# Performance work log

Measured on AMD Instinct MI355X. Metric: run time of the kernel, lower is better.

## Reference

```python
import jax, jax.numpy as jnp
import numpy as np

N_CODES = 1024
CODE_DIM = 64
COMMITMENT_WEIGHT = 0.5
DECAY = 0.99
EPSILON = 1e-05
TEMP = 1.0


def setup_inputs() -> dict:
    key = jax.random.key(0)
    k_z, k_e = jax.random.split(key)
    z = jax.random.normal(k_z, (8, 16384, CODE_DIM), dtype=jnp.float32)
    # xavier_uniform init for embedding [n_codes, code_dim]
    limit = float(np.sqrt(6.0 / (N_CODES + CODE_DIM)))
    embedding = jax.random.uniform(k_e, (N_CODES, CODE_DIM), dtype=jnp.float32,
                                   minval=-limit, maxval=limit)
    ema_cluster_size = jnp.zeros((N_CODES,), dtype=jnp.float32)
    ema_w = embedding.copy()
    return {"z": z, "embedding": embedding,
            "ema_cluster_size": ema_cluster_size, "ema_w": ema_w}


def reference(z, embedding, ema_cluster_size, ema_w):
    lead_shape = z.shape[:-1]
    zf = z.reshape(-1, z.shape[-1])  # [N, D]
    # squared-euclidean distances: ||z||^2 + ||e||^2 - 2 z e^T  -> [N, n_codes]
    d = (jnp.sum(zf * zf, axis=-1, keepdims=True)
         + jnp.sum(embedding * embedding, axis=-1)
         - 2.0 * (zf @ embedding.T)) / TEMP
    idx = jnp.argmin(d, axis=-1)  # [N]
    z_q_f = embedding[idx]        # [N, D]

    # --- EMA codebook update (no-grad buffer math) ---
    ones = jnp.ones_like(idx, dtype=zf.dtype)
    cluster_size = jax.ops.segment_sum(ones, idx, num_segments=N_CODES)      # one_hot.sum(0)
    new_ecs = ema_cluster_size * DECAY + (1.0 - DECAY) * cluster_size
    n = jnp.sum(new_ecs)
    cs = jnp.clip((new_ecs + EPSILON) / (n + N_CODES * EPSILON) * n, 0.01)
    dw = jax.ops.segment_sum(zf, idx, num_segments=N_CODES)                  # one_hot.T @ z
    new_ema_w = ema_w * DECAY + (1.0 - DECAY) * dw
    new_embedding = new_ema_w / cs[:, None]

    # --- losses (straight-through) ---
    z_q = z_q_f.reshape(z.shape)
    commitment_loss = jnp.mean((jax.lax.stop_gradient(z_q) - z) ** 2)
    codebook_loss = jnp.mean((z_q - jax.lax.stop_gradient(z)) ** 2)
    loss = commitment_loss * COMMITMENT_WEIGHT + codebook_loss
    z_q_st = z + jax.lax.stop_gradient(z_q - z)

    # --- perplexity (no-grad) ---
    avg_probs = cluster_size / jnp.sum(cluster_size)
    avg_probs = jnp.clip(avg_probs, 1e-10)
    avg_probs = avg_probs / jnp.sum(avg_probs)
    perplexity = jnp.exp(-jnp.sum(avg_probs * jnp.log(avg_probs)))

    encoding_indices = idx.reshape(lead_shape)
    return (z_q_st, encoding_indices, loss, perplexity,
            new_embedding, new_ecs, new_ema_w)
```

## Files before the change

### kernel.cpp

```cpp
#include <hip/hip_runtime.h>
#include <hip/hip_bf16.h>
#include <math.h>

#define N_ROWS   131072
#define DIMS     64
#define NCODES   1024
#define DECAY    0.99f
#define EPSF     1e-5f
#define BAND     2e-3f

#define OFF_ZQ    0
#define OFF_IDX   8388608
#define OFF_LOSS  8519680
#define OFF_PERP  8519681
#define OFF_EMB   8519682
#define OFF_ECS   8585218
#define OFF_EMAW  8586242

typedef unsigned int uint;
typedef short bf16x8 __attribute__((ext_vector_type(8)));
typedef float f32x4  __attribute__((ext_vector_type(4)));

__device__ __forceinline__ float atomic_add_f32(float* p, float v) {
  return __hip_atomic_fetch_add(p, v, __ATOMIC_RELAXED, __HIP_MEMORY_SCOPE_AGENT);
}

__device__ __forceinline__ unsigned short bf16_rne(float f) {
  uint u = __float_as_uint(f);
  uint r = u + 0x7fffu + ((u >> 16) & 1u);
  return (unsigned short)(r >> 16);
}
__device__ __forceinline__ float bf16_f32(unsigned short h) {
  return __uint_as_float(((uint)h) << 16);
}

__device__ __forceinline__ float np_pairwise64_sq(const float* v) {
#pragma clang fp contract(off)
  float r[8];
#pragma unroll
  for (int j = 0; j < 8; ++j) r[j] = v[j] * v[j];
#pragma unroll
  for (int i = 8; i < 64; i += 8)
#pragma unroll
    for (int j = 0; j < 8; ++j) r[j] += v[i + j] * v[i + j];
  return ((r[0] + r[1]) + (r[2] + r[3])) + ((r[4] + r[5]) + (r[6] + r[7]));
}

__global__ __launch_bounds__(256) void k0m(const float* __restrict__ emb,
                                           float* __restrict__ ee,
                                           uint* __restrict__ cluster,
                                           uint* __restrict__ cnt,
                                           bf16x8* __restrict__ bsplit,
                                           float* __restrict__ dw) {
  int T = blockIdx.x;
  int t = threadIdx.x;
  int gid = T * 256 + t;
  for (int i = gid; i < NCODES * DIMS; i += 16384) dw[i] = 0.0f;

  int l = t & 63;
  int slot = t >> 6;
  int ktile = slot >> 1, split = slot & 1;
  int code = T * 16 + (l & 15);
  int k0 = ktile * 32 + ((l >> 4) << 3);
  const float* ep = emb + (size_t)code * DIMS + k0;
  float4 fa = *(const float4*)ep;
  float4 fb = *(const float4*)(ep + 4);
  float fs[8] = {fa.x, fa.y, fa.z, fa.w, fb.x, fb.y, fb.z, fb.w};
  bf16x8 v;
#pragma unroll
  for (int i = 0; i < 8; ++i) {
    unsigned short h = bf16_rne(fs[i]);
    if (split == 0) v[i] = (short)h;
    else            v[i] = (short)bf16_rne(fs[i] - bf16_f32(h));
  }
  bsplit[(size_t)((T * 2 + ktile) * 2 + split) * 64 + l] = v;

  if (t < 16) {
    int c = T * 16 + t;
    float ev[DIMS];
    const float4* e4 = (const float4*)(emb + (size_t)c * DIMS);
#pragma unroll
    for (int i = 0; i < 16; ++i) {
      float4 w = e4[i];
      ev[4*i] = w.x; ev[4*i+1] = w.y; ev[4*i+2] = w.z; ev[4*i+3] = w.w;
    }
    ee[c] = np_pairwise64_sq(ev);
  } else if (t < 32) {
    cluster[T * 16 + (t - 16)] = 0u;
  }
  if (T == 0 && t == 32) *cnt = 0u;
}

__global__ __launch_bounds__(256) void k1_mfma(const float* __restrict__ z,
                                               const bf16x8* __restrict__ bsplit,
                                               const float* __restrict__ ee,
                                               int* __restrict__ idx_out,
                                               float* __restrict__ idx_f_out,
                                               uint* __restrict__ cluster,
                                               uint* __restrict__ cnt,
                                               uint* __restrict__ list) {
  int l = threadIdx.x & 63;
  int w = threadIdx.x >> 6;
  int rowbase = blockIdx.x * 64 + w * 16;
  int arow = rowbase + (l & 15);
  int kq = (l >> 4) << 3;

  bf16x8 ahi[2], ami[2];
#pragma unroll
  for (int t = 0; t < 2; ++t) {
    const float* zp = z + (size_t)arow * DIMS + t * 32 + kq;
    float4 fa = *(const float4*)zp;
    float4 fb = *(const float4*)(zp + 4);
    float fs[8] = {fa.x, fa.y, fa.z, fa.w, fb.x, fb.y, fb.z, fb.w};
#pragma unroll
    for (int i = 0; i < 8; ++i) {
      unsigned short h = bf16_rne(fs[i]);
      ahi[t][i] = (short)h;
      ami[t][i] = (short)bf16_rne(fs[i] - bf16_f32(h));
    }
  }

  float best[4]  = {3.4e38f, 3.4e38f, 3.4e38f, 3.4e38f};
  float second[4] = {3.4e38f, 3.4e38f, 3.4e38f, 3.4e38f};
  int   bidx[4] = {0, 0, 0, 0};
  int   col = l & 15;

#pragma unroll 2
  for (int T = 0; T < 64; ++T) {
    const bf16x8* bp = bsplit + (size_t)(T * 4) * 64 + l;
    bf16x8 bhi0 = bp[0];
    bf16x8 bmi0 = bp[64];
    bf16x8 bhi1 = bp[128];
    bf16x8 bmi1 = bp[192];
    f32x4 acc = {0.f, 0.f, 0.f, 0.f};
    acc = __builtin_amdgcn_mfma_f32_16x16x32_bf16(ahi[0], bhi0, acc, 0, 0, 0);
    acc = __builtin_amdgcn_mfma_f32_16x16x32_bf16(ahi[1], bhi1, acc, 0, 0, 0);
    acc = __builtin_amdgcn_mfma_f32_16x16x32_bf16(ahi[0], bmi0, acc, 0, 0, 0);
    acc = __builtin_amdgcn_mfma_f32_16x16x32_bf16(ahi[1], bmi1, acc, 0, 0, 0);
    acc = __builtin_amdgcn_mfma_f32_16x16x32_bf16(ami[0], bhi0, acc, 0, 0, 0);
    acc = __builtin_amdgcn_mfma_f32_16x16x32_bf16(ami[1], bhi1, acc, 0, 0, 0);

    int code = T * 16 + col;
    float eeT = ee[code];
#pragma unroll
    for (int j = 0; j < 4; ++j) {
      float s = fmaf(-2.0f, acc[j], eeT);
      bool lt = s < best[j];
      second[j] = lt ? best[j] : fminf(second[j], s);
      best[j]   = lt ? s : best[j];
      bidx[j]   = lt ? code : bidx[j];
    }
  }

#pragma unroll
  for (int m = 1; m < 16; m <<= 1) {
#pragma unroll
    for (int j = 0; j < 4; ++j) {
      float ob = __shfl_xor(best[j], m, 64);
      float os = __shfl_xor(second[j], m, 64);
      int   oi = __shfl_xor(bidx[j], m, 64);
      if (ob < best[j]) {
        second[j] = fminf(os, best[j]);
        best[j] = ob; bidx[j] = oi;
      } else if (ob == best[j]) {
        bidx[j] = min(bidx[j], oi);
        second[j] = fminf(second[j], fminf(os, ob));
      } else {
        second[j] = fminf(second[j], ob);
      }
    }
  }

  if (col == 0) {
#pragma unroll
    for (int j = 0; j < 4; ++j) {
      int r = rowbase + ((l >> 4) << 2) + j;
      idx_out[r] = bidx[j];
      idx_f_out[r] = (float)bidx[j];
      atomicAdd(&cluster[bidx[j]], 1u);
      if (second[j] - best[j] < BAND) {
        uint p = atomicAdd(cnt, 1u);
        list[p] = (uint)r;
      }
    }
  }
}

__global__ __launch_bounds__(256) void k2_recheck(const float* __restrict__ z,
                                                  const float* __restrict__ emb,
                                                  const float* __restrict__ ee,
                                                  const uint* __restrict__ cnt,
                                                  const uint* __restrict__ list,
                                                  int* __restrict__ idx_out,
                                                  float* __restrict__ idx_f_out,
                                                  uint* __restrict__ cluster) {
#pragma clang fp contract(off)
  __shared__ float zrow[DIMS];
  __shared__ float rv[256];
  __shared__ int   ri[256];
  int t = threadIdx.x;
  uint n = *cnt;
  for (uint i = blockIdx.x; i < n; i += gridDim.x) {
    uint row = list[i];
    __syncthreads();
    if (t < 16)
      ((float4*)zrow)[t] = ((const float4*)(z + (size_t)row * DIMS))[t];
    __syncthreads();
    float zz = np_pairwise64_sq(zrow);
    float best = 3.4e38f; int bi = 0;
#pragma unroll
    for (int k4 = 0; k4 < 4; ++k4) {
      int c = t * 4 + k4;
      const float* e = emb + (size_t)c * DIMS;
      float a = 0.f;
      for (int k = 0; k < DIMS; ++k) a = fmaf(zrow[k], e[k], a);
      float d = fmaf(-2.0f, a, zz + ee[c]);
      if (d < best) { best = d; bi = c; }
    }
    rv[t] = best; ri[t] = bi;
    __syncthreads();
    for (int s = 128; s > 0; s >>= 1) {
      if (t < s) {
        float ov = rv[t + s]; int oi = ri[t + s];
        if (ov < rv[t] || (ov == rv[t] && oi < ri[t])) { rv[t] = ov; ri[t] = oi; }
      }
      __syncthreads();
    }
    if (t == 0) {
      int old = idx_out[row];
      if (ri[0] != old) {
        atomicSub(&cluster[old], 1u);
        atomicAdd(&cluster[ri[0]], 1u);
        idx_out[row] = ri[0];
        idx_f_out[row] = (float)ri[0];
      }
    }
  }
}

__global__ __launch_bounds__(256) void k3b_prefix(const uint* __restrict__ cluster,
                                                  uint* __restrict__ starts,
                                                  uint* __restrict__ cursor) {
  __shared__ uint a[256], b[256];
  int t = threadIdx.x;
  uint c0 = cluster[t*4+0], c1 = cluster[t*4+1], c2 = cluster[t*4+2], c3 = cluster[t*4+3];
  uint s = c0 + c1 + c2 + c3;
  a[t] = s;
  __syncthreads();
  uint* src = a; uint* dst = b;
  for (int off = 1; off < 256; off <<= 1) {
    dst[t] = src[t] + ((t >= off) ? src[t - off] : 0u);
    __syncthreads();
    uint* tmp = src; src = dst; dst = tmp;
  }
  uint base = (t > 0) ? src[t-1] : 0u;
  uint p0 = base, p1 = p0 + c0, p2 = p1 + c1, p3 = p2 + c2;
  starts[t*4+0] = p0; starts[t*4+1] = p1; starts[t*4+2] = p2; starts[t*4+3] = p3;
  cursor[t*4+0] = p0; cursor[t*4+1] = p1; cursor[t*4+2] = p2; cursor[t*4+3] = p3;
  if (t == 255) starts[NCODES] = src[255];
}

__global__ __launch_bounds__(256) void k3c_scatter(const int* __restrict__ idx,
                                                   uint* __restrict__ cursor,
                                                   uint* __restrict__ rowids,
                                                   int* __restrict__ codes) {
  int row = blockIdx.x * 256 + threadIdx.x;
  int code = idx[row];
  uint pos = atomicAdd(&cursor[code], 1u);
  rowids[pos] = (uint)row;
  codes[pos] = code;
}

__global__ __launch_bounds__(256) void k3d_fused(const float* __restrict__ z,
                                                 const float* __restrict__ emb,
                                                 const uint* __restrict__ rowids,
                                                 const int* __restrict__ codes,
                                                 float* __restrict__ out_zq,
                                                 float* __restrict__ dw,
                                                 double* __restrict__ sqpart) {
  __shared__ double accd[4];
  int lane = threadIdx.x & 63, w = threadIdx.x >> 6;
  int base = blockIdx.x * 128 + w * 32;

  int cur = codes[base];
  float acc = 0.f;
  double ds = 0.0;
  for (int i = 0; i < 32; ++i) {
    int p = base + i;
    uint r = rowids[p];
    int c = codes[p];
    if (c != cur) {
      atomic_add_f32(&dw[cur * DIMS + lane], acc);
      acc = 0.f; cur = c;
    }
    float zv = z[(size_t)r * DIMS + lane];
    float ev = emb[c * DIMS + lane];
    float d = ev - zv;
    float o = zv + d;
    out_zq[(size_t)r * DIMS + lane] = o;
    acc += zv;
    ds += (double)(d * d);
  }
  atomic_add_f32(&dw[cur * DIMS + lane], acc);

#pragma unroll
  for (int o2 = 32; o2 > 0; o2 >>= 1) ds += __shfl_down(ds, o2, 64);
  if (lane == 0) accd[w] = ds;
  __syncthreads();
  if (threadIdx.x == 0)
    sqpart[blockIdx.x] = (accd[0] + accd[1]) + (accd[2] + accd[3]);
}

__global__ __launch_bounds__(256) void k4a_scalar(const float* __restrict__ ecs_in,
                                                  const uint* __restrict__ cluster,
                                                  const double* __restrict__ sqpart,
                                                  float* __restrict__ csb,
                                                  float* __restrict__ out) {
  __shared__ double red[256];
  int t = threadIdx.x;

  double nloc = 0.0, aloc = 0.0, bloc = 0.0, sloc = 0.0;
  for (int c = t; c < NCODES; c += 256) {
    float cntf = (float)cluster[c];
    float ne = ecs_in[c] * DECAY + (1.0f - DECAY) * cntf;
    out[OFF_ECS + c] = ne;
    nloc += (double)ne;
    double p = (double)cntf / (double)N_ROWS;
    double pc = p < 1e-10 ? 1e-10 : p;
    bloc += pc;
    aloc += pc * log(pc);
    sloc += sqpart[c];
  }

  red[t] = nloc; __syncthreads();
  for (int s = 128; s > 0; s >>= 1) { if (t < s) red[t] += red[t + s]; __syncthreads(); }
  double n = red[0]; __syncthreads();

  red[t] = bloc; __syncthreads();
  for (int s = 128; s > 0; s >>= 1) { if (t < s) red[t] += red[t + s]; __syncthreads(); }
  double B = red[0]; __syncthreads();

  red[t] = aloc; __syncthreads();
  for (int s = 128; s > 0; s >>= 1) { if (t < s) red[t] += red[t + s]; __syncthreads(); }
  double A = red[0]; __syncthreads();

  red[t] = sloc; __syncthreads();
  for (int s = 128; s > 0; s >>= 1) { if (t < s) red[t] += red[t + s]; __syncthreads(); }
  double S = red[0]; __syncthreads();

  if (t == 0) {
    double ent = -(A / B - log(B));
    out[OFF_PERP] = (float)exp(ent);
    double M = S / (double)((size_t)N_ROWS * DIMS);
    out[OFF_LOSS] = (float)(1.5 * M);
  }

  float nf = (float)n;
  for (int c = t; c < NCODES; c += 256) {
    float ne = out[OFF_ECS + c];
    float cs = ((ne + EPSF) / (nf + (float)NCODES * EPSF)) * nf;
    csb[c] = cs < 0.01f ? 0.01f : cs;
  }
}

__global__ __launch_bounds__(256) void k4b_emb(const float* __restrict__ emaw_in,
                                               const float* __restrict__ dw,
                                               const float* __restrict__ csb,
                                               float* __restrict__ out) {
  int i = blockIdx.x * 256 + threadIdx.x;
  int c = i >> 6;
  float nw = emaw_in[i] * DECAY + (1.0f - DECAY) * dw[i];
  out[OFF_EMAW + i] = nw;
  out[OFF_EMB + i] = nw / csb[c];
}

extern "C" void kernel_launch(void* const* d_in, const int* in_sizes, int n_in,
                              void* d_out, int out_size, void* d_ws, size_t ws_size,
                              hipStream_t stream) {
  const float* z    = (const float*)d_in[0];
  const float* emb  = (const float*)d_in[1];
  const float* ecs  = (const float*)d_in[2];
  const float* emaw = (const float*)d_in[3];
  float* out = (float*)d_out;

  char* ws = (char*)d_ws;
  uint*   cnt    = (uint*)   (ws + 0);
  int*    idxw   = (int*)    (ws + 16);
  uint*   clus   = (uint*)   (ws + 524304);
  float*  dw     = (float*)  (ws + 528416);
  float*  ee     = (float*)  (ws + 790560);
  float*  csb    = (float*)  (ws + 794656);
  uint*   starts = (uint*)   (ws + 798752);
  uint*   cursor = (uint*)   (ws + 806944);
  uint*   rowids = (uint*)   (ws + 811040);
  bf16x8* bsplit = (bf16x8*) (ws + 1335328);
  uint*   rlist  = (uint*)   (ws + 1597472);
  double* sqpart = (double*) (ws + 1597472);
  int*    codes  = (int*)    (ws + 2121760);

  k0m<<<64, 256, 0, stream>>>(emb, ee, clus, cnt, bsplit, dw);
  k1_mfma<<<N_ROWS / 64, 256, 0, stream>>>(z, bsplit, ee, idxw, out + OFF_IDX,
                                           clus, cnt, rlist);
  k2_recheck<<<1024, 256, 0, stream>>>(z, emb, ee, cnt, rlist, idxw,
                                       out + OFF_IDX, clus);
  k3b_prefix<<<1, 256, 0, stream>>>(clus, starts, cursor);
  k3c_scatter<<<N_ROWS / 256, 256, 0, stream>>>(idxw, cursor, rowids, codes);
  k3d_fused<<<N_ROWS / 128, 256, 0, stream>>>(z, emb, rowids, codes,
                                              out + OFF_ZQ, dw, sqpart);
  k4a_scalar<<<1, 256, 0, stream>>>(ecs, clus, sqpart, csb, out);
  k4b_emb<<<256, 256, 0, stream>>>(emaw, dw, csb, out);
}
```

Measured before the change: 206.1 us.

## Stage codebook tiles in LDS, fold -2 scale and norm into MFMA, merge scalar kernels

The distance kernel now stages each 16-code B tile in shared memory, with each wave loading one quarter and prefetching the next tile in registers. The -2 factor is folded into the A operands and the code norm is preloaded as the MFMA accumulator init, which removes the per-element FMA. The single-block scalar kernel is split: the EMA, perplexity and cluster-scale math moves into the prefix kernel, and the loss reduction moves into block 0 of the embedding kernel, saving one launch. This adds two block barriers per tile iteration. Scaling by -2 is exact in bf16, but adding the norm first changes the float rounding order slightly.

After: 195.4 us. 1.05x faster.

```diff
diff --git a/kernel.cpp b/kernel.cpp
--- a/kernel.cpp
+++ b/kernel.cpp
@@ -99,40 +99,54 @@
                                                uint* __restrict__ cluster,
                                                uint* __restrict__ cnt,
                                                uint* __restrict__ list) {
-  int l = threadIdx.x & 63;
-  int w = threadIdx.x >> 6;
+  __shared__ bf16x8 btile[4 * 64];
+  __shared__ float  eel[NCODES];
+  int t = threadIdx.x;
+  int l = t & 63;
+  int w = t >> 6;
   int rowbase = blockIdx.x * 64 + w * 16;
   int arow = rowbase + (l & 15);
   int kq = (l >> 4) << 3;
+  int col = l & 15;
+
+  for (int i = t; i < NCODES; i += 256) eel[i] = ee[i];
 
   bf16x8 ahi[2], ami[2];
 #pragma unroll
-  for (int t = 0; t < 2; ++t) {
-    const float* zp = z + (size_t)arow * DIMS + t * 32 + kq;
+  for (int t2 = 0; t2 < 2; ++t2) {
+    const float* zp = z + (size_t)arow * DIMS + t2 * 32 + kq;
     float4 fa = *(const float4*)zp;
     float4 fb = *(const float4*)(zp + 4);
     float fs[8] = {fa.x, fa.y, fa.z, fa.w, fb.x, fb.y, fb.z, fb.w};
 #pragma unroll
     for (int i = 0; i < 8; ++i) {
       unsigned short h = bf16_rne(fs[i]);
-      ahi[t][i] = (short)h;
-      ami[t][i] = (short)bf16_rne(fs[i] - bf16_f32(h));
+      float m = fs[i] - bf16_f32(h);
+      ahi[t2][i] = (short)bf16_rne(-2.0f * fs[i]);
+      ami[t2][i] = (short)bf16_rne(-2.0f * m);
     }
   }
 
   float best[4]  = {3.4e38f, 3.4e38f, 3.4e38f, 3.4e38f};
   float second[4] = {3.4e38f, 3.4e38f, 3.4e38f, 3.4e38f};
   int   bidx[4] = {0, 0, 0, 0};
-  int   col = l & 15;
-
-#pragma unroll 2
+
+  bf16x8 vpre = bsplit[(size_t)(0 * 4 + w) * 64 + l];
+
   for (int T = 0; T < 64; ++T) {
-    const bf16x8* bp = bsplit + (size_t)(T * 4) * 64 + l;
-    bf16x8 bhi0 = bp[0];
-    bf16x8 bmi0 = bp[64];
-    bf16x8 bhi1 = bp[128];
-    bf16x8 bmi1 = bp[192];
-    f32x4 acc = {0.f, 0.f, 0.f, 0.f};
+    __syncthreads();
+    btile[w * 64 + l] = vpre;
+    if (T < 63) vpre = bsplit[(size_t)((T + 1) * 4 + w) * 64 + l];
+    __syncthreads();
+
+    int code = T * 16 + col;
+    float eeT = eel[code];
+    bf16x8 bhi0 = btile[0 * 64 + l];
+    bf16x8 bmi0 = btile[1 * 64 + l];
+    bf16x8 bhi1 = btile[2 * 64 + l];
+    bf16x8 bmi1 = btile[3 * 64 + l];
+
+    f32x4 acc = {eeT, eeT, eeT, eeT};
     acc = __builtin_amdgcn_mfma_f32_16x16x32_bf16(ahi[0], bhi0, acc, 0, 0, 0);
     acc = __builtin_amdgcn_mfma_f32_16x16x32_bf16(ahi[1], bhi1, acc, 0, 0, 0);
     acc = __builtin_amdgcn_mfma_f32_16x16x32_bf16(ahi[0], bmi0, acc, 0, 0, 0);
@@ -140,11 +154,9 @@
     acc = __builtin_amdgcn_mfma_f32_16x16x32_bf16(ami[0], bhi0, acc, 0, 0, 0);
     acc = __builtin_amdgcn_mfma_f32_16x16x32_bf16(ami[1], bhi1, acc, 0, 0, 0);
 
-    int code = T * 16 + col;
-    float eeT = ee[code];
 #pragma unroll
     for (int j = 0; j < 4; ++j) {
-      float s = fmaf(-2.0f, acc[j], eeT);
+      float s = acc[j];
       bool lt = s < best[j];
       second[j] = lt ? best[j] : fminf(second[j], s);
       best[j]   = lt ? s : best[j];
@@ -238,14 +250,19 @@
   }
 }
 
-__global__ __launch_bounds__(256) void k3b_prefix(const uint* __restrict__ cluster,
-                                                  uint* __restrict__ starts,
-                                                  uint* __restrict__ cursor) {
+__global__ __launch_bounds__(256) void kp(const uint* __restrict__ cluster,
+                                          const float* __restrict__ ecs_in,
+                                          uint* __restrict__ starts,
+                                          uint* __restrict__ cursor,
+                                          float* __restrict__ csb,
+                                          float* __restrict__ out) {
   __shared__ uint a[256], b[256];
+  __shared__ double red[256];
   int t = threadIdx.x;
+
   uint c0 = cluster[t*4+0], c1 = cluster[t*4+1], c2 = cluster[t*4+2], c3 = cluster[t*4+3];
-  uint s = c0 + c1 + c2 + c3;
-  a[t] = s;
+  uint s4 = c0 + c1 + c2 + c3;
+  a[t] = s4;
   __syncthreads();
   uint* src = a; uint* dst = b;
   for (int off = 1; off < 256; off <<= 1) {
@@ -258,6 +275,43 @@
   starts[t*4+0] = p0; starts[t*4+1] = p1; starts[t*4+2] = p2; starts[t*4+3] = p3;
   cursor[t*4+0] = p0; cursor[t*4+1] = p1; cursor[t*4+2] = p2; cursor[t*4+3] = p3;
   if (t == 255) starts[NCODES] = src[255];
+  __syncthreads();
+
+  double nloc = 0.0, aloc = 0.0, bloc = 0.0;
+  for (int c = t; c < NCODES; c += 256) {
+    float cntf = (float)cluster[c];
+    float ne = ecs_in[c] * DECAY + (1.0f - DECAY) * cntf;
+    out[OFF_ECS + c] = ne;
+    nloc += (double)ne;
+    double p = (double)cntf / (double)N_ROWS;
+    double pc = p < 1e-10 ? 1e-10 : p;
+    bloc += pc;
+    aloc += pc * log(pc);
+  }
+
+  red[t] = nloc; __syncthreads();
+  for (int s = 128; s > 0; s >>= 1) { if (t < s) red[t] += red[t + s]; __syncthreads(); }
+  double n = red[0]; __syncthreads();
+
+  red[t] = bloc; __syncthreads();
+  for (int s = 128; s > 0; s >>= 1) { if (t < s) red[t] += red[t + s]; __syncthreads(); }
+  double B = red[0]; __syncthreads();
+
+  red[t] = aloc; __syncthreads();
+  for (int s = 128; s > 0; s >>= 1) { if (t < s) red[t] += red[t + s]; __syncthreads(); }
+  double A = red[0]; __syncthreads();
+
+  if (t == 0) {
+    double ent = -(A / B - log(B));
+    out[OFF_PERP] = (float)exp(ent);
+  }
+
+  float nf = (float)n;
+  for (int c = t; c < NCODES; c += 256) {
+    float ne = out[OFF_ECS + c];
+    float cs = ((ne + EPSF) / (nf + (float)NCODES * EPSF)) * nf;
+    csb[c] = cs < 0.01f ? 0.01f : cs;
+  }
 }
 
 __global__ __launch_bounds__(256) void k3c_scatter(const int* __restrict__ idx,
@@ -311,67 +365,29 @@
     sqpart[blockIdx.x] = (accd[0] + accd[1]) + (accd[2] + accd[3]);
 }
 
-__global__ __launch_bounds__(256) void k4a_scalar(const float* __restrict__ ecs_in,
-                                                  const uint* __restrict__ cluster,
-                                                  const double* __restrict__ sqpart,
-                                                  float* __restrict__ csb,
-                                                  float* __restrict__ out) {
-  __shared__ double red[256];
-  int t = threadIdx.x;
-
-  double nloc = 0.0, aloc = 0.0, bloc = 0.0, sloc = 0.0;
-  for (int c = t; c < NCODES; c += 256) {
-    float cntf = (float)cluster[c];
-    float ne = ecs_in[c] * DECAY + (1.0f - DECAY) * cntf;
-    out[OFF_ECS + c] = ne;
-    nloc += (double)ne;
-    double p = (double)cntf / (double)N_ROWS;
-    double pc = p < 1e-10 ? 1e-10 : p;
-    bloc += pc;
-    aloc += pc * log(pc);
-    sloc += sqpart[c];
-  }
-
-  red[t] = nloc; __syncthreads();
-  for (int s = 128; s > 0; s >>= 1) { if (t < s) red[t] += red[t + s]; __syncthreads(); }
-  double n = red[0]; __syncthreads();
-
-  red[t] = bloc; __syncthreads();
-  for (int s = 128; s > 0; s >>= 1) { if (t < s) red[t] += red[t + s]; __syncthreads(); }
-  double B = red[0]; __syncthreads();
-
-  red[t] = aloc; __syncthreads();
-  for (int s = 128; s > 0; s >>= 1) { if (t < s) red[t] += red[t + s]; __syncthreads(); }
-  double A = red[0]; __syncthreads();
-
-  red[t] = sloc; __syncthreads();
-  for (int s = 128; s > 0; s >>= 1) { if (t < s) red[t] += red[t + s]; __syncthreads(); }
-  double S = red[0]; __syncthreads();
-
-  if (t == 0) {
-    double ent = -(A / B - log(B));
-    out[OFF_PERP] = (float)exp(ent);
-    double M = S / (double)((size_t)N_ROWS * DIMS);
-    out[OFF_LOSS] = (float)(1.5 * M);
-  }
-
-  float nf = (float)n;
-  for (int c = t; c < NCODES; c += 256) {
-    float ne = out[OFF_ECS + c];
-    float cs = ((ne + EPSF) / (nf + (float)NCODES * EPSF)) * nf;
-    csb[c] = cs < 0.01f ? 0.01f : cs;
-  }
-}
-
 __global__ __launch_bounds__(256) void k4b_emb(const float* __restrict__ emaw_in,
                                                const float* __restrict__ dw,
                                                const float* __restrict__ csb,
+                                               const double* __restrict__ sqpart,
                                                float* __restrict__ out) {
   int i = blockIdx.x * 256 + threadIdx.x;
   int c = i >> 6;
   float nw = emaw_in[i] * DECAY + (1.0f - DECAY) * dw[i];
   out[OFF_EMAW + i] = nw;
   out[OFF_EMB + i] = nw / csb[c];
+
+  if (blockIdx.x == 0) {
+    __shared__ double red[256];
+    int t = threadIdx.x;
+    double sloc = 0.0;
+    for (int k = t; k < 1024; k += 256) sloc += sqpart[k];
+    red[t] = sloc; __syncthreads();
+    for (int s = 128; s > 0; s >>= 1) { if (t < s) red[t] += red[t + s]; __syncthreads(); }
+    if (t == 0) {
+      double M = red[0] / (double)((size_t)N_ROWS * DIMS);
+      out[OFF_LOSS] = (float)(1.5 * M);
+    }
+  }
 }
 
 extern "C" void kernel_launch(void* const* d_in, const int* in_sizes, int n_in,
@@ -403,10 +419,9 @@
                                            clus, cnt, rlist);
   k2_recheck<<<1024, 256, 0, stream>>>(z, emb, ee, cnt, rlist, idxw,
                                        out + OFF_IDX, clus);
-  k3b_prefix<<<1, 256, 0, stream>>>(clus, starts, cursor);
+  kp<<<1, 256, 0, stream>>>(clus, ecs, starts, cursor, csb, out);
   k3c_scatter<<<N_ROWS / 256, 256, 0, stream>>>(idxw, cursor, rowids, codes);
   k3d_fused<<<N_ROWS / 128, 256, 0, stream>>>(z, emb, rowids, codes,
                                               out + OFF_ZQ, dw, sqpart);
-  k4a_scalar<<<1, 256, 0, stream>>>(ecs, clus, sqpart, csb, out);
-  k4b_emb<<<256, 256, 0, stream>>>(emaw, dw, csb, out);
-}
+  k4b_emb<<<256, 256, 0, stream>>>(emaw, dw, csb, sqpart, out);
+}
```
